# Optimization experiments

Measured on AMD Instinct MI355X. Metric: run time of the kernel, lower is better.

Reference implementation:

```python
import jax, jax.numpy as jnp
import numpy as np

B, S, D = 32, 4096, 1024
NEG = -1e37


def setup_inputs() -> dict:
    key = jax.random.key(0)
    k1, k2, k3, k4 = jax.random.split(key, 4)
    keys = jax.random.normal(k1, (B, S, D), dtype=jnp.float32)
    queries = jax.random.normal(k2, (B, 1, D), dtype=jnp.float32)
    values = jax.random.normal(k3, (B, S, D), dtype=jnp.float32)
    mask = jax.random.randint(k4, (B, S), 0, 2) > 0
    # guarantee at least one valid position per row so softmax is well-defined
    mask = mask.at[:, 0].set(True)
    return {"keys": keys, "queries": queries, "values": values, "mask": mask}


def reference(keys, queries, values, mask):
    # attention_logits: [B, 1, S] = queries @ keys^T
    logits = jnp.einsum("bqd,bkd->bqk", queries, keys)
    # custom masking with -1e37 (not -inf), matching torch.where semantics
    logits = jnp.where(mask[:, None, :], logits, jnp.float32(NEG))
    attn = jax.nn.softmax(logits, axis=-1)  # [B, 1, S]
    out = jnp.einsum("bqk,bkd->bqd", attn, values)  # [B, 1, D]
    return out
```

## Files before the change

### kernel.cpp

```cpp
#include <hip/hip_runtime.h>

#define BATCH 32
#define SEQ   4096
#define DIM   1024
#define NEGV  (-1e37f)
#define SPLIT 32
#define ROWS_PER_BLOCK 64

__global__ __launch_bounds__(256) void qk_logits(
    const float* __restrict__ K, const float* __restrict__ Q,
    const int* __restrict__ mask, float* __restrict__ logits) {
  const int b    = blockIdx.x;
  const int s0   = blockIdx.y * ROWS_PER_BLOCK;
  const int tid  = threadIdx.x;
  const int lane = tid & 63;
  const int wave = tid >> 6;

  const float4* q4 = (const float4*)(Q + (size_t)b * DIM);
  const float4 q0 = q4[lane];
  const float4 q1 = q4[64 + lane];
  const float4 q2 = q4[128 + lane];
  const float4 q3 = q4[192 + lane];

  const int rows_per_wave = ROWS_PER_BLOCK / 4;
  for (int r = 0; r < rows_per_wave; ++r) {
    const int s = s0 + wave * rows_per_wave + r;
    if (mask[(size_t)b * SEQ + s] == 0) {
      if (lane == 0) logits[(size_t)b * SEQ + s] = NEGV;
      continue;
    }
    const float4* k4 = (const float4*)(K + ((size_t)b * SEQ + s) * DIM);
    const float4 k0 = k4[lane];
    const float4 k1 = k4[64 + lane];
    const float4 k2 = k4[128 + lane];
    const float4 k3 = k4[192 + lane];
    float acc = q0.x*k0.x + q0.y*k0.y + q0.z*k0.z + q0.w*k0.w;
    acc      += q1.x*k1.x + q1.y*k1.y + q1.z*k1.z + q1.w*k1.w;
    acc      += q2.x*k2.x + q2.y*k2.y + q2.z*k2.z + q2.w*k2.w;
    acc      += q3.x*k3.x + q3.y*k3.y + q3.z*k3.z + q3.w*k3.w;
    for (int off = 32; off > 0; off >>= 1)
      acc += __shfl_down(acc, off, 64);
    if (lane == 0) logits[(size_t)b * SEQ + s] = acc;
  }
}

__global__ __launch_bounds__(256) void softmax_w(float* __restrict__ lw) {
  const int b   = blockIdx.x;
  const int tid = threadIdx.x;
  const int lane = tid & 63;
  const int wave = tid >> 6;
  __shared__ float wmax[4];
  __shared__ float wsum[4];

  float lv[16];
  float lm = -3.4e38f;
  #pragma unroll
  for (int i = 0; i < 16; ++i) {
    lv[i] = lw[(size_t)b * SEQ + tid + i * 256];
    lm = fmaxf(lm, lv[i]);
  }
  for (int off = 32; off > 0; off >>= 1)
    lm = fmaxf(lm, __shfl_down(lm, off, 64));
  if (lane == 0) wmax[wave] = lm;
  __syncthreads();
  const float m = fmaxf(fmaxf(wmax[0], wmax[1]), fmaxf(wmax[2], wmax[3]));

  float e[16];
  float ls = 0.f;
  #pragma unroll
  for (int i = 0; i < 16; ++i) {
    e[i] = __expf(lv[i] - m);
    ls += e[i];
  }
  for (int off = 32; off > 0; off >>= 1)
    ls += __shfl_down(ls, off, 64);
  if (lane == 0) wsum[wave] = ls;
  __syncthreads();
  const float inv = 1.0f / (wsum[0] + wsum[1] + wsum[2] + wsum[3]);
  #pragma unroll
  for (int i = 0; i < 16; ++i)
    lw[(size_t)b * SEQ + tid + i * 256] = e[i] * inv;
}

__global__ __launch_bounds__(256) void wv_partial(
    const float* __restrict__ V, const float* __restrict__ w,
    float* __restrict__ part) {
  const int b   = blockIdx.x;
  const int c   = blockIdx.y;
  const int tid = threadIdx.x;
  const int s0  = c * (SEQ / SPLIT);
  float4 acc = make_float4(0.f, 0.f, 0.f, 0.f);
  for (int i = 0; i < SEQ / SPLIT; ++i) {
    const int s = s0 + i;
    const float wi = w[(size_t)b * SEQ + s];
    if (wi != 0.0f) {
      const float4 v = ((const float4*)(V + ((size_t)b * SEQ + s) * DIM))[tid];
      acc.x += wi * v.x; acc.y += wi * v.y; acc.z += wi * v.z; acc.w += wi * v.w;
    }
  }
  ((float4*)(part + ((size_t)b * SPLIT + c) * DIM))[tid] = acc;
}

__global__ __launch_bounds__(256) void reduce_out(
    const float* __restrict__ part, float* __restrict__ out) {
  const int b   = blockIdx.x;
  const int tid = threadIdx.x;
  float4 acc = make_float4(0.f, 0.f, 0.f, 0.f);
  for (int c = 0; c < SPLIT; ++c) {
    const float4 p = ((const float4*)(part + ((size_t)b * SPLIT + c) * DIM))[tid];
    acc.x += p.x; acc.y += p.y; acc.z += p.z; acc.w += p.w;
  }
  ((float4*)(out + (size_t)b * DIM))[tid] = acc;
}

extern "C" void kernel_launch(void* const* d_in, const int* in_sizes, int n_in,
                              void* d_out, int out_size, void* d_ws, size_t ws_size,
                              hipStream_t stream) {
  const float* keys    = (const float*)d_in[0];
  const float* queries = (const float*)d_in[1];
  const float* values  = (const float*)d_in[2];
  const int*   mask    = (const int*)d_in[3];
  float* out = (float*)d_out;

  float* lw   = (float*)d_ws;
  float* part = lw + (size_t)BATCH * SEQ;

  qk_logits<<<dim3(BATCH, SEQ / ROWS_PER_BLOCK), 256, 0, stream>>>(keys, queries, mask, lw);
  softmax_w<<<BATCH, 256, 0, stream>>>(lw);
  wv_partial<<<dim3(BATCH, SPLIT), 256, 0, stream>>>(values, lw, part);
  reduce_out<<<BATCH, 256, 0, stream>>>(part, out);
}
```

Measured before the change: 866.7 us.

## Fuse QK, softmax and weighted V into split-K flash-decoding with combine

Replaces the four-kernel pipeline (logits, softmax, weighted V partials, reduce) with two kernels. Each block now computes logits for a 64-row chunk into shared memory, takes a local max, and accumulates exp-weighted V rows along with a local sum. A combine kernel then rescales the partials by the global max. This removes the logits round-trip through global memory and two launches, and raises V-pass parallelism from 32 to 64 chunks per batch. The cost is a larger partial buffer and an extra rescale pass in the combine step.

```diff
diff --git a/kernel.cpp b/kernel.cpp
--- a/kernel.cpp
+++ b/kernel.cpp
@@ -1,20 +1,28 @@
 #include <hip/hip_runtime.h>
 
-#define BATCH 32
-#define SEQ   4096
-#define DIM   1024
-#define NEGV  (-1e37f)
-#define SPLIT 32
-#define ROWS_PER_BLOCK 64
+#define BATCH  32
+#define SEQ    4096
+#define DIM    1024
+#define NEGV   (-1e37f)
+#define NCHUNK 64
+#define CHUNK  (SEQ / NCHUNK)
+#define RPW    (CHUNK / 4)
 
-__global__ __launch_bounds__(256) void qk_logits(
+__global__ __launch_bounds__(256) void attn_partial(
     const float* __restrict__ K, const float* __restrict__ Q,
-    const int* __restrict__ mask, float* __restrict__ logits) {
+    const float* __restrict__ V, const int* __restrict__ mask,
+    float* __restrict__ part, float* __restrict__ ml) {
   const int b    = blockIdx.x;
-  const int s0   = blockIdx.y * ROWS_PER_BLOCK;
+  const int c    = blockIdx.y;
+  const int s0   = c * CHUNK;
   const int tid  = threadIdx.x;
   const int lane = tid & 63;
   const int wave = tid >> 6;
+
+  __shared__ float slog[CHUNK];
+
+  const int mv = mask[(size_t)b * SEQ + s0 + lane];
+  const unsigned long long bm = __ballot(mv != 0);
 
   const float4* q4 = (const float4*)(Q + (size_t)b * DIM);
   const float4 q0 = q4[lane];
@@ -22,14 +30,13 @@
   const float4 q2 = q4[128 + lane];
   const float4 q3 = q4[192 + lane];
 
-  const int rows_per_wave = ROWS_PER_BLOCK / 4;
-  for (int r = 0; r < rows_per_wave; ++r) {
-    const int s = s0 + wave * rows_per_wave + r;
-    if (mask[(size_t)b * SEQ + s] == 0) {
-      if (lane == 0) logits[(size_t)b * SEQ + s] = NEGV;
+  for (int r = 0; r < RPW; ++r) {
+    const int li = wave * RPW + r;
+    if (!((bm >> li) & 1ull)) {
+      if (lane == 0) slog[li] = NEGV;
       continue;
     }
-    const float4* k4 = (const float4*)(K + ((size_t)b * SEQ + s) * DIM);
+    const float4* k4 = (const float4*)(K + ((size_t)b * SEQ + s0 + li) * DIM);
     const float4 k0 = k4[lane];
     const float4 k1 = k4[64 + lane];
     const float4 k2 = k4[128 + lane];
@@ -40,76 +47,58 @@
     acc      += q3.x*k3.x + q3.y*k3.y + q3.z*k3.z + q3.w*k3.w;
     for (int off = 32; off > 0; off >>= 1)
       acc += __shfl_down(acc, off, 64);
-    if (lane == 0) logits[(size_t)b * SEQ + s] = acc;
+    if (lane == 0) slog[li] = acc;
   }
+  __syncthreads();
+
+  float m = NEGV;
+  #pragma unroll
+  for (int i = 0; i < CHUNK; ++i) m = fmaxf(m, slog[i]);
+
+  float4 acc = make_float4(0.f, 0.f, 0.f, 0.f);
+  float lsum = 0.f;
+  for (int i = 0; i < CHUNK; ++i) {
+    const float l = slog[i];
+    if (l == NEGV) continue;
+    const float e = __expf(l - m);
+    lsum += e;
+    const float4 v = ((const float4*)(V + ((size_t)b * SEQ + s0 + i) * DIM))[tid];
+    acc.x += e * v.x; acc.y += e * v.y; acc.z += e * v.z; acc.w += e * v.w;
+  }
+
+  ((float4*)(part + ((size_t)b * NCHUNK + c) * DIM))[tid] = acc;
+  if (tid == 0)
+    ((float2*)ml)[(size_t)b * NCHUNK + c] = make_float2(m, lsum);
 }
 
-__global__ __launch_bounds__(256) void softmax_w(float* __restrict__ lw) {
+__global__ __launch_bounds__(256) void attn_combine(
+    const float* __restrict__ part, const float* __restrict__ ml,
+    float* __restrict__ out) {
   const int b   = blockIdx.x;
   const int tid = threadIdx.x;
-  const int lane = tid & 63;
-  const int wave = tid >> 6;
-  __shared__ float wmax[4];
-  __shared__ float wsum[4];
+  __shared__ float sm[NCHUNK];
+  __shared__ float sl[NCHUNK];
+  if (tid < NCHUNK) {
+    const float2 v = ((const float2*)ml)[(size_t)b * NCHUNK + tid];
+    sm[tid] = v.x;
+    sl[tid] = v.y;
+  }
+  __syncthreads();
 
-  float lv[16];
-  float lm = -3.4e38f;
+  float M = -3.4e38f;
   #pragma unroll
-  for (int i = 0; i < 16; ++i) {
-    lv[i] = lw[(size_t)b * SEQ + tid + i * 256];
-    lm = fmaxf(lm, lv[i]);
+  for (int i = 0; i < NCHUNK; ++i) M = fmaxf(M, sm[i]);
+
+  float4 acc = make_float4(0.f, 0.f, 0.f, 0.f);
+  float denom = 0.f;
+  for (int cc = 0; cc < NCHUNK; ++cc) {
+    const float sc = __expf(sm[cc] - M);
+    denom += sc * sl[cc];
+    const float4 p = ((const float4*)(part + ((size_t)b * NCHUNK + cc) * DIM))[tid];
+    acc.x += sc * p.x; acc.y += sc * p.y; acc.z += sc * p.z; acc.w += sc * p.w;
   }
-  for (int off = 32; off > 0; off >>= 1)
-    lm = fmaxf(lm, __shfl_down(lm, off, 64));
-  if (lane == 0) wmax[wave] = lm;
-  __syncthreads();
-  const float m = fmaxf(fmaxf(wmax[0], wmax[1]), fmaxf(wmax[2], wmax[3]));
-
-  float e[16];
-  float ls = 0.f;
-  #pragma unroll
-  for (int i = 0; i < 16; ++i) {
-    e[i] = __expf(lv[i] - m);
-    ls += e[i];
-  }
-  for (int off = 32; off > 0; off >>= 1)
-    ls += __shfl_down(ls, off, 64);
-  if (lane == 0) wsum[wave] = ls;
-  __syncthreads();
-  const float inv = 1.0f / (wsum[0] + wsum[1] + wsum[2] + wsum[3]);
-  #pragma unroll
-  for (int i = 0; i < 16; ++i)
-    lw[(size_t)b * SEQ + tid + i * 256] = e[i] * inv;
-}
-
-__global__ __launch_bounds__(256) void wv_partial(
-    const float* __restrict__ V, const float* __restrict__ w,
-    float* __restrict__ part) {
-  const int b   = blockIdx.x;
-  const int c   = blockIdx.y;
-  const int tid = threadIdx.x;
-  const int s0  = c * (SEQ / SPLIT);
-  float4 acc = make_float4(0.f, 0.f, 0.f, 0.f);
-  for (int i = 0; i < SEQ / SPLIT; ++i) {
-    const int s = s0 + i;
-    const float wi = w[(size_t)b * SEQ + s];
-    if (wi != 0.0f) {
-      const float4 v = ((const float4*)(V + ((size_t)b * SEQ + s) * DIM))[tid];
-      acc.x += wi * v.x; acc.y += wi * v.y; acc.z += wi * v.z; acc.w += wi * v.w;
-    }
-  }
-  ((float4*)(part + ((size_t)b * SPLIT + c) * DIM))[tid] = acc;
-}
-
-__global__ __launch_bounds__(256) void reduce_out(
-    const float* __restrict__ part, float* __restrict__ out) {
-  const int b   = blockIdx.x;
-  const int tid = threadIdx.x;
-  float4 acc = make_float4(0.f, 0.f, 0.f, 0.f);
-  for (int c = 0; c < SPLIT; ++c) {
-    const float4 p = ((const float4*)(part + ((size_t)b * SPLIT + c) * DIM))[tid];
-    acc.x += p.x; acc.y += p.y; acc.z += p.z; acc.w += p.w;
-  }
+  const float inv = 1.0f / denom;
+  acc.x *= inv; acc.y *= inv; acc.z *= inv; acc.w *= inv;
   ((float4*)(out + (size_t)b * DIM))[tid] = acc;
 }
 
@@ -122,11 +111,9 @@
   const int*   mask    = (const int*)d_in[3];
   float* out = (float*)d_out;
 
-  float* lw   = (float*)d_ws;
-  float* part = lw + (size_t)BATCH * SEQ;
+  float* part = (float*)d_ws;
+  float* ml   = part + (size_t)BATCH * NCHUNK * DIM;
 
-  qk_logits<<<dim3(BATCH, SEQ / ROWS_PER_BLOCK), 256, 0, stream>>>(keys, queries, mask, lw);
-  softmax_w<<<BATCH, 256, 0, stream>>>(lw);
-  wv_partial<<<dim3(BATCH, SPLIT), 256, 0, stream>>>(values, lw, part);
-  reduce_out<<<BATCH, 256, 0, stream>>>(part, out);
+  attn_partial<<<dim3(BATCH, NCHUNK), 256, 0, stream>>>(keys, queries, values, mask, part, ml);
+  attn_combine<<<BATCH, 256, 0, stream>>>(part, ml, out);
 }
```

Result: slower. 899.7 us (+3.8%).
